# Kernel optimization log

Measured on AMD Instinct MI355X. Metric: run time of the kernel, lower is better.

## Reference

```python
import jax, jax.numpy as jnp
import numpy as np

HID = 1024
INTER = 4096
NUM_EXPERTS = 4096
NUM_KEYS = 64  # floor(sqrt(4096))
TOP_K = 8
B, S = 2, 2048


def setup_inputs() -> dict:
    key = jax.random.key(0)
    ks = jax.random.split(key, 7)
    sc = 0.02
    return {
        "hidden_states": jax.random.normal(ks[0], (B, S, HID), jnp.float32),
        "w_gate": jax.random.normal(ks[1], (INTER, HID), jnp.float32) * sc,
        "w_up": jax.random.normal(ks[2], (INTER, HID), jnp.float32) * sc,
        "w_down": jax.random.normal(ks[3], (HID, INTER), jnp.float32) * sc,
        "w_router": jax.random.normal(ks[4], (NUM_KEYS * 2, HID), jnp.float32) * sc,
        "down_embed": jax.random.normal(ks[5], (NUM_EXPERTS, HID), jnp.float32) * sc,
        "up_embed": jax.random.normal(ks[6], (NUM_EXPERTS, HID), jnp.float32) * sc,
    }


def reference(hidden_states, w_gate, w_up, w_down, w_router, down_embed, up_embed):
    b, s, h = hidden_states.shape
    n = b * s
    # router: [b,s,2*nk] -> row-major reshape to (2, n, nk), matching torch .view
    router_logits = (hidden_states @ w_router.T).reshape(2, n, NUM_KEYS)
    # topk with k == nk is a full descending sort (faithful to torch .topk)
    scores_xy, idx_xy = jax.lax.top_k(router_logits, NUM_KEYS)
    scores_x, scores_y = scores_xy[0], scores_xy[1]  # (n, nk) each
    idx_x, idx_y = idx_xy[0], idx_xy[1]
    all_scores = (scores_x[:, :, None] + scores_y[:, None, :]).reshape(n, NUM_KEYS * NUM_KEYS)
    all_indices = (idx_x[:, :, None] * NUM_KEYS + idx_y[:, None, :]).reshape(n, NUM_KEYS * NUM_KEYS)
    scores, pos = jax.lax.top_k(all_scores, TOP_K)  # (n, top_k)
    indices = jnp.take_along_axis(all_indices, pos, axis=-1)
    routing_weights = jax.nn.softmax(scores, axis=-1)
    routing_weights = routing_weights / routing_weights.sum(-1, keepdims=True)  # norm_topk_prob
    de = down_embed[indices]  # (n, top_k, h)
    ue = up_embed[indices]    # (n, top_k, h)
    x_flat = hidden_states.reshape(n, h)
    ew = jnp.einsum('nkh,nh->nk', de, x_flat)
    ew = jax.nn.silu(ew) * routing_weights
    experts_states = jnp.einsum('nk,nkh->nh', ew, ue).reshape(b, s, h)
    mlp = (jax.nn.silu(x_flat @ w_gate.T) * (x_flat @ w_up.T)) @ w_down.T
    out = mlp.reshape(b, s, h) + experts_states
    return (out, router_logits)
```

## Files before the change

kernel.cpp:

```cpp
#include <hip/hip_runtime.h>
#include <hip/hip_bf16.h>
#include <stdint.h>

typedef __bf16 bf16;
typedef __attribute__((ext_vector_type(8))) __bf16 bf16x8;
typedef __attribute__((ext_vector_type(4))) float f32x4;

static constexpr int kTok = 4096;
static constexpr int kHid = 1024;
static constexpr int kInter = 4096;

#define GLDS16(g, l)                                                \
  __builtin_amdgcn_global_load_lds(                                 \
      (const __attribute__((address_space(1))) void*)(g),           \
      (__attribute__((address_space(3))) void*)(l), 16, 0, 0)

__global__ void __launch_bounds__(256) k_cvt_all(
    const float* X, const float* Wg, const float* Wu, const float* Wd,
    const float* Wr, bf16* Xb, bf16* Wgb, bf16* Wub, bf16* Wdb, bf16* Wrb) {
  const float* src;
  bf16* dst;
  long n;
  switch (blockIdx.y) {
    case 0: src = X;  dst = Xb;  n = (long)kTok * kHid;   break;
    case 1: src = Wg; dst = Wgb; n = (long)kInter * kHid; break;
    case 2: src = Wu; dst = Wub; n = (long)kInter * kHid; break;
    case 3: src = Wd; dst = Wdb; n = (long)kHid * kInter; break;
    default: src = Wr; dst = Wrb; n = 128L * kHid;        break;
  }
  const long i = ((long)blockIdx.x * 256 + threadIdx.x) * 8;
  if (i >= n) return;
  const f32x4 a = *(const f32x4*)(src + i);
  const f32x4 b = *(const f32x4*)(src + i + 4);
  bf16x8 o;
#pragma unroll
  for (int k = 0; k < 4; ++k) { o[k] = (bf16)a[k]; o[4 + k] = (bf16)b[k]; }
  *(bf16x8*)(dst + i) = o;
}

__global__ void __launch_bounds__(256, 2) gemm_router(
    const bf16* A, const bf16* Bm, float* outF) {
  constexpr int K = kHid, N = 128;
  __shared__ bf16 sA[128 * 32];
  __shared__ bf16 sB[128 * 32];
  const int t = threadIdx.x;
  const int w = t >> 6;
  const int L = t & 63;
  const long m0 = (long)blockIdx.y * 128;
  const int zb = blockIdx.z * 256;
  const int wm = (w >> 1) * 64;
  const int wn = (w & 1) * 64;

  f32x4 acc[4][4];
  const f32x4 fzero = {0.f, 0.f, 0.f, 0.f};
#pragma unroll
  for (int i = 0; i < 4; ++i)
#pragma unroll
    for (int j = 0; j < 4; ++j) acc[i][j] = fzero;

  const int r0 = t >> 2;
  const int ko = (t & 3) * 8;
  const bf16* gA0 = A + (m0 + r0) * K + zb + ko;
  const bf16* gA1 = gA0 + (long)64 * K;
  const bf16* gB0 = Bm + (long)r0 * K + zb + ko;
  const bf16* gB1 = gB0 + (long)64 * K;
  bf16* lA0 = sA + w * 512;
  bf16* lA1 = sA + 2048 + w * 512;
  bf16* lB0 = sB + w * 512;
  bf16* lB1 = sB + 2048 + w * 512;

  const int la = L & 15;
  const int lk = (L >> 4) * 8;
  const bf16* sAr = sA + (wm + la) * 32 + lk;
  const bf16* sBr = sB + (wn + la) * 32 + lk;

  for (int kt = 0; kt < 8; ++kt) {
    const int k0 = kt << 5;
    GLDS16(gA0 + k0, lA0);
    GLDS16(gA1 + k0, lA1);
    GLDS16(gB0 + k0, lB0);
    GLDS16(gB1 + k0, lB1);
    __syncthreads();
    bf16x8 af[4], bfm[4];
#pragma unroll
    for (int i = 0; i < 4; ++i) {
      af[i] = *(const bf16x8*)(sAr + i * 16 * 32);
      bfm[i] = *(const bf16x8*)(sBr + i * 16 * 32);
    }
#pragma unroll
    for (int i = 0; i < 4; ++i)
#pragma unroll
      for (int j = 0; j < 4; ++j)
        acc[i][j] = __builtin_amdgcn_mfma_f32_16x16x32_bf16(af[i], bfm[j],
                                                            acc[i][j], 0, 0, 0);
    __syncthreads();
  }
  const long col0 = wn + la;
  const long row0 = m0 + wm + (L >> 4) * 4;
#pragma unroll
  for (int i = 0; i < 4; ++i)
#pragma unroll
    for (int j = 0; j < 4; ++j)
#pragma unroll
      for (int r = 0; r < 4; ++r)
        __hip_atomic_fetch_add(&outF[(row0 + i * 16 + r) * N + col0 + j * 16],
                               acc[i][j][r], __ATOMIC_RELAXED,
                               __HIP_MEMORY_SCOPE_AGENT);
}

__global__ void __launch_bounds__(256, 2) gemm_gu(
    const bf16* X, const bf16* Wg, const bf16* Wu, bf16* H) {
  constexpr int K = kHid, N = kInter;
  __shared__ bf16 sX[128 * 32];
  __shared__ bf16 sG[128 * 32];
  __shared__ bf16 sU[128 * 32];
  const int t = threadIdx.x;
  const int w = t >> 6;
  const int L = t & 63;
  const long m0 = (long)blockIdx.y * 128;
  const long n0 = (long)blockIdx.x * 128;
  const int wm = (w >> 1) * 64;
  const int wn = (w & 1) * 64;

  f32x4 accG[4][4], accU[4][4];
  const f32x4 fzero = {0.f, 0.f, 0.f, 0.f};
#pragma unroll
  for (int i = 0; i < 4; ++i)
#pragma unroll
    for (int j = 0; j < 4; ++j) { accG[i][j] = fzero; accU[i][j] = fzero; }

  const int r0 = t >> 2;
  const int ko = (t & 3) * 8;
  const bf16* gX0 = X + (m0 + r0) * K + ko;
  const bf16* gX1 = gX0 + (long)64 * K;
  const bf16* gG0 = Wg + (n0 + r0) * K + ko;
  const bf16* gG1 = gG0 + (long)64 * K;
  const bf16* gU0 = Wu + (n0 + r0) * K + ko;
  const bf16* gU1 = gU0 + (long)64 * K;
  bf16* lX0 = sX + w * 512;
  bf16* lX1 = sX + 2048 + w * 512;
  bf16* lG0 = sG + w * 512;
  bf16* lG1 = sG + 2048 + w * 512;
  bf16* lU0 = sU + w * 512;
  bf16* lU1 = sU + 2048 + w * 512;

  const int la = L & 15;
  const int lk = (L >> 4) * 8;
  const bf16* sXr = sX + (wm + la) * 32 + lk;
  const bf16* sGr = sG + (wn + la) * 32 + lk;
  const bf16* sUr = sU + (wn + la) * 32 + lk;

  for (int kt = 0; kt < K / 32; ++kt) {
    const int k0 = kt << 5;
    GLDS16(gX0 + k0, lX0);
    GLDS16(gX1 + k0, lX1);
    GLDS16(gG0 + k0, lG0);
    GLDS16(gG1 + k0, lG1);
    GLDS16(gU0 + k0, lU0);
    GLDS16(gU1 + k0, lU1);
    __syncthreads();
    bf16x8 af[4], bg[4], bu[4];
#pragma unroll
    for (int i = 0; i < 4; ++i) {
      af[i] = *(const bf16x8*)(sXr + i * 16 * 32);
      bg[i] = *(const bf16x8*)(sGr + i * 16 * 32);
      bu[i] = *(const bf16x8*)(sUr + i * 16 * 32);
    }
#pragma unroll
    for (int i = 0; i < 4; ++i)
#pragma unroll
      for (int j = 0; j < 4; ++j) {
        accG[i][j] = __builtin_amdgcn_mfma_f32_16x16x32_bf16(af[i], bg[j],
                                                             accG[i][j], 0, 0, 0);
        accU[i][j] = __builtin_amdgcn_mfma_f32_16x16x32_bf16(af[i], bu[j],
                                                             accU[i][j], 0, 0, 0);
      }
    __syncthreads();
  }
  const long col0 = n0 + wn + la;
  const long row0 = m0 + wm + (L >> 4) * 4;
#pragma unroll
  for (int i = 0; i < 4; ++i)
#pragma unroll
    for (int j = 0; j < 4; ++j)
#pragma unroll
      for (int r = 0; r < 4; ++r) {
        const float g = accG[i][j][r];
        const float u = accU[i][j][r];
        H[(row0 + i * 16 + r) * N + col0 + j * 16] =
            (bf16)(g / (1.f + __expf(-g)) * u);
      }
}

__global__ void __launch_bounds__(256, 2) gemm_down(
    const bf16* Hs, const bf16* Wd, float* out0) {
  constexpr int K = kInter, N = kHid;
  __shared__ bf16 sA[128 * 32];
  __shared__ bf16 sB[128 * 32];
  const int t = threadIdx.x;
  const int w = t >> 6;
  const int L = t & 63;
  const long m0 = (long)blockIdx.y * 128;
  const long n0 = (long)blockIdx.x * 128;
  const long zb = (long)blockIdx.z * 2048;
  const int wm = (w >> 1) * 64;
  const int wn = (w & 1) * 64;

  f32x4 acc[4][4];
  const f32x4 fzero = {0.f, 0.f, 0.f, 0.f};
#pragma unroll
  for (int i = 0; i < 4; ++i)
#pragma unroll
    for (int j = 0; j < 4; ++j) acc[i][j] = fzero;

  const int r0 = t >> 2;
  const int ko = (t & 3) * 8;
  const bf16* gA0 = Hs + (m0 + r0) * K + zb + ko;
  const bf16* gA1 = gA0 + (long)64 * K;
  const bf16* gB0 = Wd + (n0 + r0) * K + zb + ko;
  const bf16* gB1 = gB0 + (long)64 * K;
  bf16* lA0 = sA + w * 512;
  bf16* lA1 = sA + 2048 + w * 512;
  bf16* lB0 = sB + w * 512;
  bf16* lB1 = sB + 2048 + w * 512;

  const int la = L & 15;
  const int lk = (L >> 4) * 8;
  const bf16* sAr = sA + (wm + la) * 32 + lk;
  const bf16* sBr = sB + (wn + la) * 32 + lk;

  for (int kt = 0; kt < 64; ++kt) {
    const int k0 = kt << 5;
    GLDS16(gA0 + k0, lA0);
    GLDS16(gA1 + k0, lA1);
    GLDS16(gB0 + k0, lB0);
    GLDS16(gB1 + k0, lB1);
    __syncthreads();
    bf16x8 af[4], bfm[4];
#pragma unroll
    for (int i = 0; i < 4; ++i) {
      af[i] = *(const bf16x8*)(sAr + i * 16 * 32);
      bfm[i] = *(const bf16x8*)(sBr + i * 16 * 32);
    }
#pragma unroll
    for (int i = 0; i < 4; ++i)
#pragma unroll
      for (int j = 0; j < 4; ++j)
        acc[i][j] = __builtin_amdgcn_mfma_f32_16x16x32_bf16(af[i], bfm[j],
                                                            acc[i][j], 0, 0, 0);
    __syncthreads();
  }
  const long col0 = n0 + wn + la;
  const long row0 = m0 + wm + (L >> 4) * 4;
#pragma unroll
  for (int i = 0; i < 4; ++i)
#pragma unroll
    for (int j = 0; j < 4; ++j)
#pragma unroll
      for (int r = 0; r < 4; ++r)
        __hip_atomic_fetch_add(
            &out0[(row0 + i * 16 + r) * N + col0 + j * 16], acc[i][j][r],
            __ATOMIC_RELAXED, __HIP_MEMORY_SCOPE_AGENT);
}

__global__ void k_zero4(float* p) {
  const long i = ((long)blockIdx.x * 256 + threadIdx.x) * 4;
  const f32x4 z = {0.f, 0.f, 0.f, 0.f};
  *(f32x4*)(p + i) = z;
}

__global__ void __launch_bounds__(256) route_expert(
    const float* logits, const float* X, const float* dE, const float* uE,
    float* out0) {
  __shared__ float s_vals[4][128];
  __shared__ int s_idx[4][128];
  const int w = threadIdx.x >> 6;
  const int L = threadIdx.x & 63;
  const int j = blockIdx.x * 4 + w;

  const int half = (j & 1) * 64;
  const int rx = j >> 1;
  const float vx = logits[(long)rx * 128 + half + L];
  const float vy = logits[(long)(2048 + rx) * 128 + half + L];

  int rkx = 0, rky = 0;
  for (int m = 0; m < 64; ++m) {
    const float mx = __shfl(vx, m);
    const float my = __shfl(vy, m);
    rkx += (mx > vx) || (mx == vx && m < L);
    rky += (my > vy) || (my == vy && m < L);
  }
  rkx &= 63;
  rky &= 63;
  s_vals[w][rkx] = vx;
  s_idx[w][rkx] = L;
  s_vals[w][64 + rky] = vy;
  s_idx[w][64 + rky] = L;
  __syncthreads();

  int p = 0, q = 0;
  const bool valid = (L < 20);
  if (L < 8)       { p = L;      q = 0; }
  else if (L < 12) { p = L - 8;  q = 1; }
  else if (L < 14) { p = L - 12; q = 2; }
  else if (L < 16) { p = L - 14; q = 3; }
  else if (L < 20) { p = 0;      q = L - 12; }
  const float kNegBig = -3.0e38f;
  float myv = valid ? (s_vals[w][p] + s_vals[w][64 + q]) : kNegBig;
  int mypos = valid ? (p * 64 + q) : 0x7fffffff;

  float topv[8];
  int tope[8];
#pragma unroll
  for (int r = 0; r < 8; ++r) {
    float bv = myv;
    int bp = mypos;
#pragma unroll
    for (int d = 32; d > 0; d >>= 1) {
      const float ov = __shfl_xor(bv, d);
      const int op = __shfl_xor(bp, d);
      if (ov > bv || (ov == bv && op < bp)) { bv = ov; bp = op; }
    }
    topv[r] = bv;
    const int pp = (bp >> 6) & 127, qq = bp & 63;
    tope[r] = (s_idx[w][pp] * 64 + s_idx[w][64 + qq]) & 4095;
    if (mypos == bp) myv = kNegBig;
  }

  float e[8], wsum = 0.f;
#pragma unroll
  for (int r = 0; r < 8; ++r) {
    e[r] = __expf(topv[r] - topv[0]);
    wsum += e[r];
  }
  const float winv = 1.f / wsum;

  const long xoff = (long)j * kHid + L * 16;
  float xv[16], acc[16];
#pragma unroll
  for (int v4 = 0; v4 < 4; ++v4) {
    const f32x4 xl = *(const f32x4*)(X + xoff + v4 * 4);
#pragma unroll
    for (int i = 0; i < 4; ++i) { xv[v4 * 4 + i] = xl[i]; acc[v4 * 4 + i] = 0.f; }
  }

  for (int r = 0; r < 8; ++r) {
    const long eo = (long)tope[r] * kHid + L * 16;
    float d = 0.f;
#pragma unroll
    for (int v4 = 0; v4 < 4; ++v4) {
      const f32x4 dl = *(const f32x4*)(dE + eo + v4 * 4);
#pragma unroll
      for (int i = 0; i < 4; ++i) d += dl[i] * xv[v4 * 4 + i];
    }
#pragma unroll
    for (int dd = 32; dd > 0; dd >>= 1) d += __shfl_xor(d, dd);
    const float ew = d / (1.f + __expf(-d)) * (e[r] * winv);
#pragma unroll
    for (int v4 = 0; v4 < 4; ++v4) {
      const f32x4 ul = *(const f32x4*)(uE + eo + v4 * 4);
#pragma unroll
      for (int i = 0; i < 4; ++i) acc[v4 * 4 + i] += ew * ul[i];
    }
  }

  float* po = out0 + xoff;
#pragma unroll
  for (int v4 = 0; v4 < 4; ++v4) {
    f32x4 ov = *(const f32x4*)(po + v4 * 4);
#pragma unroll
    for (int i = 0; i < 4; ++i) ov[i] += acc[v4 * 4 + i];
    *(f32x4*)(po + v4 * 4) = ov;
  }
}

extern "C" void kernel_launch(void* const* d_in, const int* in_sizes, int n_in,
                              void* d_out, int out_size, void* d_ws,
                              size_t ws_size, hipStream_t stream) {
  (void)in_sizes; (void)n_in; (void)out_size; (void)ws_size;
  const float* X  = (const float*)d_in[0];
  const float* Wg = (const float*)d_in[1];
  const float* Wu = (const float*)d_in[2];
  const float* Wd = (const float*)d_in[3];
  const float* Wr = (const float*)d_in[4];
  const float* dE = (const float*)d_in[5];
  const float* uE = (const float*)d_in[6];

  float* out0 = (float*)d_out;
  float* out1 = out0 + (size_t)kTok * kHid;

  bf16* wsH = (bf16*)d_ws;
  bf16* Wrb = wsH;
  bf16* Xb  = wsH + (size_t)kTok * kInter;
  bf16* Wgb = Xb  + (size_t)kTok * kHid;
  bf16* Wub = Wgb + (size_t)kInter * kHid;
  bf16* Wdb = Wub + (size_t)kInter * kHid;

  dim3 blk(256);
  k_zero4<<<dim3((kTok * kHid + 2 * kTok * 64) / 1024), blk, 0, stream>>>(out0);
  k_cvt_all<<<dim3(2048, 5), blk, 0, stream>>>(X, Wg, Wu, Wd, Wr,
                                               Xb, Wgb, Wub, Wdb, Wrb);
  gemm_router<<<dim3(1, 32, 4), blk, 0, stream>>>(Xb, Wrb, out1);
  gemm_gu<<<dim3(32, 32), blk, 0, stream>>>(Xb, Wgb, Wub, wsH);
  gemm_down<<<dim3(8, 32, 2), blk, 0, stream>>>(wsH, Wdb, out0);
  route_expert<<<dim3(kTok / 4), blk, 0, stream>>>(out1, X, dE, uE, out0);
}
```

Baseline: 346.6 us.

## Replace split-K atomics with smaller output tiles and direct stores

The router and down-projection GEMMs no longer split K across blocks and accumulate with atomics. Instead they use narrower output tiles (64-row or 64-col) so there are still enough blocks, and each block writes its result directly. This removes the zeroing kernel and the atomic read-modify-write traffic on the outputs. The cost is lower per-block arithmetic intensity and more redundant loading of the shared operand. The route_expert kernel still accumulates into out0, which works only if it adds onto the values gemm_down has already stored.

```diff
diff --git a/kernel.cpp b/kernel.cpp
--- a/kernel.cpp
+++ b/kernel.cpp
@@ -18,6 +18,7 @@
 __global__ void __launch_bounds__(256) k_cvt_all(
     const float* X, const float* Wg, const float* Wu, const float* Wd,
     const float* Wr, bf16* Xb, bf16* Wgb, bf16* Wub, bf16* Wdb, bf16* Wrb) {
+  const long i = ((long)blockIdx.x * 256 + threadIdx.x) * 8;
   const float* src;
   bf16* dst;
   long n;
@@ -28,7 +29,6 @@
     case 3: src = Wd; dst = Wdb; n = (long)kHid * kInter; break;
     default: src = Wr; dst = Wrb; n = 128L * kHid;        break;
   }
-  const long i = ((long)blockIdx.x * 256 + threadIdx.x) * 8;
   if (i >= n) return;
   const f32x4 a = *(const f32x4*)(src + i);
   const f32x4 b = *(const f32x4*)(src + i + 4);
@@ -41,31 +41,28 @@
 __global__ void __launch_bounds__(256, 2) gemm_router(
     const bf16* A, const bf16* Bm, float* outF) {
   constexpr int K = kHid, N = 128;
-  __shared__ bf16 sA[128 * 32];
+  __shared__ bf16 sA[64 * 32];
   __shared__ bf16 sB[128 * 32];
   const int t = threadIdx.x;
   const int w = t >> 6;
   const int L = t & 63;
-  const long m0 = (long)blockIdx.y * 128;
-  const int zb = blockIdx.z * 256;
-  const int wm = (w >> 1) * 64;
+  const long m0 = (long)blockIdx.x * 64;
+  const int wm = (w >> 1) * 32;
   const int wn = (w & 1) * 64;
 
-  f32x4 acc[4][4];
+  f32x4 acc[2][4];
   const f32x4 fzero = {0.f, 0.f, 0.f, 0.f};
 #pragma unroll
-  for (int i = 0; i < 4; ++i)
+  for (int i = 0; i < 2; ++i)
 #pragma unroll
     for (int j = 0; j < 4; ++j) acc[i][j] = fzero;
 
   const int r0 = t >> 2;
   const int ko = (t & 3) * 8;
-  const bf16* gA0 = A + (m0 + r0) * K + zb + ko;
-  const bf16* gA1 = gA0 + (long)64 * K;
-  const bf16* gB0 = Bm + (long)r0 * K + zb + ko;
+  const bf16* gA0 = A + (m0 + r0) * K + ko;
+  const bf16* gB0 = Bm + (long)r0 * K + ko;
   const bf16* gB1 = gB0 + (long)64 * K;
   bf16* lA0 = sA + w * 512;
-  bf16* lA1 = sA + 2048 + w * 512;
   bf16* lB0 = sB + w * 512;
   bf16* lB1 = sB + 2048 + w * 512;
 
@@ -74,21 +71,19 @@
   const bf16* sAr = sA + (wm + la) * 32 + lk;
   const bf16* sBr = sB + (wn + la) * 32 + lk;
 
-  for (int kt = 0; kt < 8; ++kt) {
-    const int k0 = kt << 5;
+  for (int kt = 0; kt < K / 32; ++kt) {
+    const long k0 = (long)kt << 5;
     GLDS16(gA0 + k0, lA0);
-    GLDS16(gA1 + k0, lA1);
     GLDS16(gB0 + k0, lB0);
     GLDS16(gB1 + k0, lB1);
     __syncthreads();
-    bf16x8 af[4], bfm[4];
-#pragma unroll
-    for (int i = 0; i < 4; ++i) {
-      af[i] = *(const bf16x8*)(sAr + i * 16 * 32);
-      bfm[i] = *(const bf16x8*)(sBr + i * 16 * 32);
-    }
-#pragma unroll
-    for (int i = 0; i < 4; ++i)
+    bf16x8 af[2], bfm[4];
+#pragma unroll
+    for (int i = 0; i < 2; ++i) af[i] = *(const bf16x8*)(sAr + i * 512);
+#pragma unroll
+    for (int j = 0; j < 4; ++j) bfm[j] = *(const bf16x8*)(sBr + j * 512);
+#pragma unroll
+    for (int i = 0; i < 2; ++i)
 #pragma unroll
       for (int j = 0; j < 4; ++j)
         acc[i][j] = __builtin_amdgcn_mfma_f32_16x16x32_bf16(af[i], bfm[j],
@@ -98,14 +93,12 @@
   const long col0 = wn + la;
   const long row0 = m0 + wm + (L >> 4) * 4;
 #pragma unroll
-  for (int i = 0; i < 4; ++i)
+  for (int i = 0; i < 2; ++i)
 #pragma unroll
     for (int j = 0; j < 4; ++j)
 #pragma unroll
       for (int r = 0; r < 4; ++r)
-        __hip_atomic_fetch_add(&outF[(row0 + i * 16 + r) * N + col0 + j * 16],
-                               acc[i][j][r], __ATOMIC_RELAXED,
-                               __HIP_MEMORY_SCOPE_AGENT);
+        outF[(row0 + i * 16 + r) * N + col0 + j * 16] = acc[i][j][r];
 }
 
 __global__ void __launch_bounds__(256, 2) gemm_gu(
@@ -151,7 +144,7 @@
   const bf16* sUr = sU + (wn + la) * 32 + lk;
 
   for (int kt = 0; kt < K / 32; ++kt) {
-    const int k0 = kt << 5;
+    const long k0 = (long)kt << 5;
     GLDS16(gX0 + k0, lX0);
     GLDS16(gX1 + k0, lX1);
     GLDS16(gG0 + k0, lG0);
@@ -162,9 +155,9 @@
     bf16x8 af[4], bg[4], bu[4];
 #pragma unroll
     for (int i = 0; i < 4; ++i) {
-      af[i] = *(const bf16x8*)(sXr + i * 16 * 32);
-      bg[i] = *(const bf16x8*)(sGr + i * 16 * 32);
-      bu[i] = *(const bf16x8*)(sUr + i * 16 * 32);
+      af[i] = *(const bf16x8*)(sXr + i * 512);
+      bg[i] = *(const bf16x8*)(sGr + i * 512);
+      bu[i] = *(const bf16x8*)(sUr + i * 512);
     }
 #pragma unroll
     for (int i = 0; i < 4; ++i)
@@ -196,56 +189,51 @@
     const bf16* Hs, const bf16* Wd, float* out0) {
   constexpr int K = kInter, N = kHid;
   __shared__ bf16 sA[128 * 32];
-  __shared__ bf16 sB[128 * 32];
+  __shared__ bf16 sB[64 * 32];
   const int t = threadIdx.x;
   const int w = t >> 6;
   const int L = t & 63;
   const long m0 = (long)blockIdx.y * 128;
-  const long n0 = (long)blockIdx.x * 128;
-  const long zb = (long)blockIdx.z * 2048;
+  const long n0 = (long)blockIdx.x * 64;
   const int wm = (w >> 1) * 64;
-  const int wn = (w & 1) * 64;
-
-  f32x4 acc[4][4];
+  const int wn = (w & 1) * 32;
+
+  f32x4 acc[4][2];
   const f32x4 fzero = {0.f, 0.f, 0.f, 0.f};
 #pragma unroll
   for (int i = 0; i < 4; ++i)
 #pragma unroll
-    for (int j = 0; j < 4; ++j) acc[i][j] = fzero;
+    for (int j = 0; j < 2; ++j) acc[i][j] = fzero;
 
   const int r0 = t >> 2;
   const int ko = (t & 3) * 8;
-  const bf16* gA0 = Hs + (m0 + r0) * K + zb + ko;
+  const bf16* gA0 = Hs + (m0 + r0) * K + ko;
   const bf16* gA1 = gA0 + (long)64 * K;
-  const bf16* gB0 = Wd + (n0 + r0) * K + zb + ko;
-  const bf16* gB1 = gB0 + (long)64 * K;
+  const bf16* gB0 = Wd + (n0 + r0) * K + ko;
   bf16* lA0 = sA + w * 512;
   bf16* lA1 = sA + 2048 + w * 512;
   bf16* lB0 = sB + w * 512;
-  bf16* lB1 = sB + 2048 + w * 512;
 
   const int la = L & 15;
   const int lk = (L >> 4) * 8;
   const bf16* sAr = sA + (wm + la) * 32 + lk;
   const bf16* sBr = sB + (wn + la) * 32 + lk;
 
-  for (int kt = 0; kt < 64; ++kt) {
-    const int k0 = kt << 5;
+  for (int kt = 0; kt < K / 32; ++kt) {
+    const long k0 = (long)kt << 5;
     GLDS16(gA0 + k0, lA0);
     GLDS16(gA1 + k0, lA1);
     GLDS16(gB0 + k0, lB0);
-    GLDS16(gB1 + k0, lB1);
-    __syncthreads();
-    bf16x8 af[4], bfm[4];
-#pragma unroll
-    for (int i = 0; i < 4; ++i) {
-      af[i] = *(const bf16x8*)(sAr + i * 16 * 32);
-      bfm[i] = *(const bf16x8*)(sBr + i * 16 * 32);
-    }
+    __syncthreads();
+    bf16x8 af[4], bfm[2];
+#pragma unroll
+    for (int i = 0; i < 4; ++i) af[i] = *(const bf16x8*)(sAr + i * 512);
+#pragma unroll
+    for (int j = 0; j < 2; ++j) bfm[j] = *(const bf16x8*)(sBr + j * 512);
 #pragma unroll
     for (int i = 0; i < 4; ++i)
 #pragma unroll
-      for (int j = 0; j < 4; ++j)
+      for (int j = 0; j < 2; ++j)
         acc[i][j] = __builtin_amdgcn_mfma_f32_16x16x32_bf16(af[i], bfm[j],
                                                             acc[i][j], 0, 0, 0);
     __syncthreads();
@@ -255,18 +243,10 @@
 #pragma unroll
   for (int i = 0; i < 4; ++i)
 #pragma unroll
-    for (int j = 0; j < 4; ++j)
+    for (int j = 0; j < 2; ++j)
 #pragma unroll
       for (int r = 0; r < 4; ++r)
-        __hip_atomic_fetch_add(
-            &out0[(row0 + i * 16 + r) * N + col0 + j * 16], acc[i][j][r],
-            __ATOMIC_RELAXED, __HIP_MEMORY_SCOPE_AGENT);
-}
-
-__global__ void k_zero4(float* p) {
-  const long i = ((long)blockIdx.x * 256 + threadIdx.x) * 4;
-  const f32x4 z = {0.f, 0.f, 0.f, 0.f};
-  *(f32x4*)(p + i) = z;
+        out0[(row0 + i * 16 + r) * N + col0 + j * 16] = acc[i][j][r];
 }
 
 __global__ void __launch_bounds__(256) route_expert(
@@ -397,11 +377,10 @@
   bf16* Wdb = Wub + (size_t)kInter * kHid;
 
   dim3 blk(256);
-  k_zero4<<<dim3((kTok * kHid + 2 * kTok * 64) / 1024), blk, 0, stream>>>(out0);
   k_cvt_all<<<dim3(2048, 5), blk, 0, stream>>>(X, Wg, Wu, Wd, Wr,
                                                Xb, Wgb, Wub, Wdb, Wrb);
-  gemm_router<<<dim3(1, 32, 4), blk, 0, stream>>>(Xb, Wrb, out1);
+  gemm_router<<<dim3(64), blk, 0, stream>>>(Xb, Wrb, out1);
   gemm_gu<<<dim3(32, 32), blk, 0, stream>>>(Xb, Wgb, Wub, wsH);
-  gemm_down<<<dim3(8, 32, 2), blk, 0, stream>>>(wsH, Wdb, out0);
+  gemm_down<<<dim3(16, 32), blk, 0, stream>>>(wsH, Wdb, out0);
   route_expert<<<dim3(kTok / 4), blk, 0, stream>>>(out1, X, dE, uE, out0);
 }
```

After: 348.9 us. No clear change (+0.7%).
